# Kernel optimization log

Measured on AMD Instinct MI355X. Metric: run time of the kernel, lower is better.

The kernel has to match this reference:

```python
import jax, jax.numpy as jnp
import numpy as np

B, S, HID = 4, 2048, 2048
H, KV, D = 16, 4, 128
G = H // KV  # kv groups
EPS = 1e-6
SCALE = D ** -0.5


def setup_inputs() -> dict:
    key = jax.random.key(0)
    ks = jax.random.split(key, 8)
    hidden_states = jax.random.normal(ks[0], (B, S, HID), jnp.float32)
    # real RoPE tables (rotate-half convention: freqs duplicated across halves)
    inv_freq = 1.0 / (10000.0 ** (np.arange(0, D, 2, dtype=np.float32) / D))
    t = np.arange(S, dtype=np.float32)
    freqs = np.outer(t, inv_freq)                      # [S, D/2]
    emb = np.concatenate([freqs, freqs], axis=-1)      # [S, D]
    cos = jnp.asarray(np.cos(emb), jnp.float32)
    sin = jnp.asarray(np.sin(emb), jnp.float32)
    std = HID ** -0.5
    Wq = jax.random.normal(ks[1], (HID, H * D), jnp.float32) * std
    Wk = jax.random.normal(ks[2], (HID, KV * D), jnp.float32) * std
    Wv = jax.random.normal(ks[3], (HID, KV * D), jnp.float32) * std
    Wo = jax.random.normal(ks[4], (H * D, HID), jnp.float32) * std
    q_norm_w = jnp.ones((D,), jnp.float32)
    k_norm_w = jnp.ones((D,), jnp.float32)
    return {"hidden_states": hidden_states, "cos": cos, "sin": sin,
            "Wq": Wq, "Wk": Wk, "Wv": Wv, "Wo": Wo,
            "q_norm_w": q_norm_w, "k_norm_w": k_norm_w}


def _rms_norm(x, w):
    xf = x.astype(jnp.float32)
    var = jnp.mean(xf * xf, axis=-1, keepdims=True)
    return w * (xf * jax.lax.rsqrt(var + EPS)).astype(x.dtype)


def _rotate_half(x):
    x1, x2 = x[..., : D // 2], x[..., D // 2:]
    return jnp.concatenate([-x2, x1], axis=-1)


def reference(hidden_states, cos, sin, Wq, Wk, Wv, Wo, q_norm_w, k_norm_w):
    x = hidden_states  # [B, S, HID]
    # projections + per-head RMSNorm
    q = _rms_norm((x @ Wq).reshape(B, S, H, D), q_norm_w).transpose(0, 2, 1, 3)   # [B,H,S,D]
    k = _rms_norm((x @ Wk).reshape(B, S, KV, D), k_norm_w).transpose(0, 2, 1, 3)  # [B,KV,S,D]
    v = (x @ Wv).reshape(B, S, KV, D).transpose(0, 2, 1, 3)                        # [B,KV,S,D]
    # RoPE (cos/sin broadcast [S,D] -> [B,heads,S,D])
    q = q * cos + _rotate_half(q) * sin
    k = k * cos + _rotate_half(k) * sin
    # GQA attention without materializing expanded K/V: group q heads per kv head
    qg = q.reshape(B, KV, G, S, D)
    scores = jnp.einsum('bkgsd,bktd->bkgst', qg, k) * SCALE       # [B,KV,G,S,S]
    probs = jax.nn.softmax(scores, axis=-1)
    out = jnp.einsum('bkgst,bktd->bkgsd', probs, v)               # [B,KV,G,S,D]
    out = out.reshape(B, H, S, D).transpose(0, 2, 1, 3).reshape(B, S, H * D)
    return out @ Wo
```

## Files before the change

### kernel.cpp

```cpp
#include <hip/hip_runtime.h>

#define DEVI __device__ __forceinline__

#define B_    4
#define S_    2048
#define HID_  2048
#define H_    16
#define KV_   4
#define D_    128
#define NQKV_ 3072
#define SCALE_ 0.08838834764831845f
#define L2E_   1.44269504088896340736f

typedef __bf16 bf16x8 __attribute__((ext_vector_type(8)));
typedef float  f32x4  __attribute__((ext_vector_type(4)));
typedef unsigned short ushort_t;

DEVI unsigned short f2bu(float f) {
  unsigned u = __float_as_uint(f);
  u += 0x7fffu + ((u >> 16) & 1u);
  return (unsigned short)(u >> 16);
}
DEVI float bu2f(unsigned short s) { return __uint_as_float(((unsigned)s) << 16); }

DEVI void storev(ushort_t* p, float v) { *p = f2bu(v); }
DEVI void storev(float* p, float v)    { *p = v; }

DEVI void gl_lds16(const void* gptr, void* ldsptr) {
  __builtin_amdgcn_global_load_lds(
      (const __attribute__((address_space(1))) void*)gptr,
      (__attribute__((address_space(3))) void*)ldsptr, 16, 0, 0);
}

__global__ void k_cvt(const float* __restrict__ in, ushort_t* __restrict__ out, int n8) {
  int i = blockIdx.x * blockDim.x + threadIdx.x;
  if (i >= n8) return;
  const float4* p = (const float4*)in + (size_t)i * 2;
  float4 a = p[0], b = p[1];
  uint4 o;
  o.x = (unsigned)f2bu(a.x) | ((unsigned)f2bu(a.y) << 16);
  o.y = (unsigned)f2bu(a.z) | ((unsigned)f2bu(a.w) << 16);
  o.z = (unsigned)f2bu(b.x) | ((unsigned)f2bu(b.y) << 16);
  o.w = (unsigned)f2bu(b.z) | ((unsigned)f2bu(b.w) << 16);
  ((uint4*)out)[i] = o;
}

__global__ void k_transw(const float* __restrict__ in, ushort_t* __restrict__ out,
                         int K, int N) {
  __shared__ float tile[64][65];
  int k0 = blockIdx.x * 64, n0 = blockIdx.y * 64;
  int c = threadIdx.x & 63, r0 = threadIdx.x >> 6;
  #pragma unroll
  for (int i = 0; i < 16; ++i) {
    int r = r0 * 16 + i;
    tile[r][c] = in[(size_t)(k0 + r) * N + n0 + c];
  }
  __syncthreads();
  #pragma unroll
  for (int i = 0; i < 16; ++i) {
    int r = r0 * 16 + i;
    out[(size_t)(n0 + r) * K + k0 + c] = f2bu(tile[c][r]);
  }
}

template <typename OutT>
__global__ __launch_bounds__(256)
void k_gemm(const ushort_t* __restrict__ A, const ushort_t* __restrict__ Bt,
            OutT* __restrict__ C, int M, int N, int K) {
  __shared__ __align__(16) ushort_t As[128 * 64];
  __shared__ __align__(16) ushort_t Bs[128 * 64];
  const int tid = threadIdx.x;
  const int wave = tid >> 6, lane = tid & 63;
  const int wr = wave >> 1, wc = wave & 1;
  const int h4 = lane >> 4, c16 = lane & 15;
  const int m0 = blockIdx.x * 128, n0 = blockIdx.y * 128;

  const int srow  = wave * 8 + (lane >> 3);
  const int scolb = (lane & 7) * 16;

  const ushort_t* Ap = A  + (size_t)m0 * K;
  const ushort_t* Bp = Bt + (size_t)n0 * K;

  f32x4 acc[4][4] = {};

  for (int kt = 0; kt < K; kt += 64) {
    __syncthreads();
    #pragma unroll
    for (int p = 0; p < 4; ++p) {
      int row = p * 32 + srow;
      gl_lds16((const char*)(Ap + (size_t)row * K + kt) + scolb,
               (char*)As + p * 4096 + wave * 1024);
      gl_lds16((const char*)(Bp + (size_t)row * K + kt) + scolb,
               (char*)Bs + p * 4096 + wave * 1024);
    }
    __syncthreads();
    #pragma unroll
    for (int kc = 0; kc < 2; ++kc) {
      bf16x8 af[4], bfr[4];
      #pragma unroll
      for (int m = 0; m < 4; ++m)
        af[m] = *(const bf16x8*)((const char*)As + (wr * 64 + m * 16 + c16) * 128 + kc * 64 + h4 * 16);
      #pragma unroll
      for (int n = 0; n < 4; ++n)
        bfr[n] = *(const bf16x8*)((const char*)Bs + (wc * 64 + n * 16 + c16) * 128 + kc * 64 + h4 * 16);
      #pragma unroll
      for (int m = 0; m < 4; ++m)
        #pragma unroll
        for (int n = 0; n < 4; ++n)
          acc[m][n] = __builtin_amdgcn_mfma_f32_16x16x32_bf16(af[m], bfr[n], acc[m][n], 0, 0, 0);
    }
  }
  #pragma unroll
  for (int m = 0; m < 4; ++m)
    #pragma unroll
    for (int n = 0; n < 4; ++n)
      #pragma unroll
      for (int r = 0; r < 4; ++r) {
        int grow = m0 + wr * 64 + m * 16 + h4 * 4 + r;
        int gcol = n0 + wc * 64 + n * 16 + c16;
        storev(&C[(size_t)grow * N + gcol], acc[m][n][r]);
      }
}

__global__ void k_normrope(const ushort_t* __restrict__ qkv,
                           const float* __restrict__ cosT, const float* __restrict__ sinT,
                           const float* __restrict__ qw, const float* __restrict__ kw,
                           ushort_t* __restrict__ Qr,
                           ushort_t* __restrict__ Kr,
                           ushort_t* __restrict__ Vt) {
  int wid = blockIdx.x * 4 + (threadIdx.x >> 6);
  int lane = threadIdx.x & 63;
  int sub = wid % 24;
  int bs = wid / 24;
  int b = bs >> 11, s = bs & 2047;
  if (sub < 20) {
    bool isQ = sub < 16;
    int head = isQ ? sub : sub - 16;
    const ushort_t* rp = qkv + (size_t)bs * NQKV_ + (isQ ? head * 128 : 2048 + head * 128);
    float e0 = bu2f(rp[lane]);
    float e1 = bu2f(rp[lane + 64]);
    float ss2 = e0 * e0 + e1 * e1;
    #pragma unroll
    for (int off = 32; off; off >>= 1) ss2 += __shfl_xor(ss2, off);
    float rinv = rsqrtf(ss2 * (1.0f / 128.0f) + 1e-6f);
    const float* w = isQ ? qw : kw;
    float y0 = e0 * rinv * w[lane];
    float y1 = e1 * rinv * w[lane + 64];
    float c0 = cosT[s * 128 + lane],      sn0 = sinT[s * 128 + lane];
    float c1 = cosT[s * 128 + lane + 64], sn1 = sinT[s * 128 + lane + 64];
    float o0 = y0 * c0 - y1 * sn0;
    float o1 = y1 * c1 + y0 * sn1;
    if (isQ) { o0 *= SCALE_; o1 *= SCALE_; }
    ushort_t* op = isQ ? (Qr + ((size_t)(b * H_ + head) * S_ + s) * D_)
                       : (Kr + ((size_t)(b * KV_ + head) * S_ + s) * D_);
    op[lane]      = f2bu(o0);
    op[lane + 64] = f2bu(o1);
  } else {
    int vh = sub - 20;
    const ushort_t* rp = qkv + (size_t)bs * NQKV_ + 2560 + vh * 128;
    ushort_t* op = Vt + ((size_t)(b * KV_ + vh) * D_) * S_ + s;
    op[(size_t)lane * S_]        = rp[lane];
    op[(size_t)(lane + 64) * S_] = rp[lane + 64];
  }
}

__global__ __launch_bounds__(256)
void k_attn(const ushort_t* __restrict__ Qr, const ushort_t* __restrict__ Kr,
            const ushort_t* __restrict__ Vt, ushort_t* __restrict__ AO) {
  __shared__ __align__(16) ushort_t Ks[64 * 128];
  __shared__ __align__(16) ushort_t Vs[128 * 64];
  __shared__ __align__(16) ushort_t Ps[4][16 * 64];
  const int bh = blockIdx.y;
  const int b = bh >> 4, h = bh & 15, kvh = h >> 2;
  const int q0 = blockIdx.x * 64;
  const int tid = threadIdx.x;
  const int wave = tid >> 6, lane = tid & 63;
  const int h4 = lane >> 4, c16 = lane & 15;

  const ushort_t* qp = Qr + ((size_t)(b * H_ + h) * S_ + q0 + wave * 16 + c16) * D_;
  bf16x8 qf[4];
  #pragma unroll
  for (int kc = 0; kc < 4; ++kc)
    qf[kc] = *(const bf16x8*)(qp + kc * 32 + h4 * 8);

  const ushort_t* Kg = Kr + (size_t)(b * KV_ + kvh) * S_ * D_;
  const ushort_t* Vg = Vt + (size_t)(b * KV_ + kvh) * D_ * S_;

  float mrow = -1e30f, lsum = 0.0f;
  f32x4 Of[8] = {};
  ushort_t* pw = &Ps[wave][0];
  const int xq = (c16 & 7) << 4;

  for (int nt = 0; nt < S_ / 64; ++nt) {
    const int s0 = nt * 64;
    __syncthreads();
    #pragma unroll
    for (int p = 0; p < 4; ++p) {
      int off = p * 4096 + wave * 1024 + lane * 16;
      {
        int row = off >> 8, colb = off & 255;
        int sc = colb ^ ((row & 7) << 4);
        gl_lds16((const char*)(Kg + (size_t)(s0 + row) * D_) + sc,
                 (char*)Ks + p * 4096 + wave * 1024);
      }
      {
        int row = off >> 7, colb = off & 127;
        int sc = colb ^ ((row & 7) << 4);
        gl_lds16((const char*)(Vg + (size_t)row * S_ + s0) + sc,
                 (char*)Vs + p * 4096 + wave * 1024);
      }
    }
    __syncthreads();

    f32x4 st[4] = {};
    #pragma unroll
    for (int kvt = 0; kvt < 4; ++kvt) {
      const int krow = kvt * 16 + c16;
      const int xr = (krow & 7) << 4;
      #pragma unroll
      for (int kc = 0; kc < 4; ++kc) {
        bf16x8 kf = *(const bf16x8*)((const char*)Ks + krow * 256 + ((kc * 64 + h4 * 16) ^ xr));
        st[kvt] = __builtin_amdgcn_mfma_f32_16x16x32_bf16(kf, qf[kc], st[kvt], 0, 0, 0);
      }
    }

    float tmax = -1e30f;
    #pragma unroll
    for (int kvt = 0; kvt < 4; ++kvt)
      #pragma unroll
      for (int r = 0; r < 4; ++r) tmax = fmaxf(tmax, st[kvt][r]);
    tmax = fmaxf(tmax, __shfl_xor(tmax, 16));
    tmax = fmaxf(tmax, __shfl_xor(tmax, 32));
    const float mnew = fmaxf(mrow, tmax);
    const float corr = exp2f((mrow - mnew) * L2E_);
    mrow = mnew;

    float psum = 0.0f;
    #pragma unroll
    for (int kvt = 0; kvt < 4; ++kvt)
      #pragma unroll
      for (int r = 0; r < 4; ++r) {
        float pv = exp2f((st[kvt][r] - mnew) * L2E_);
        psum += pv;
        int kvi = kvt * 16 + h4 * 4 + r;
        *(ushort_t*)((char*)pw + c16 * 128 + ((kvi * 2) ^ xq)) = f2bu(pv);
      }
    lsum = lsum * corr + psum;

    float cr[4];
    #pragma unroll
    for (int r = 0; r < 4; ++r) cr[r] = __shfl(corr, (lane & 48) + h4 * 4 + r);
    #pragma unroll
    for (int dt = 0; dt < 8; ++dt)
      #pragma unroll
      for (int r = 0; r < 4; ++r) Of[dt][r] *= cr[r];

    #pragma unroll
    for (int kvc = 0; kvc < 2; ++kvc) {
      bf16x8 pa = *(const bf16x8*)((const char*)pw + c16 * 128 + ((kvc * 64 + h4 * 16) ^ xq));
      #pragma unroll
      for (int dt = 0; dt < 8; ++dt) {
        const int vrow = dt * 16 + c16;
        bf16x8 vb = *(const bf16x8*)((const char*)Vs + vrow * 128 +
                                     ((kvc * 64 + h4 * 16) ^ ((vrow & 7) << 4)));
        Of[dt] = __builtin_amdgcn_mfma_f32_16x16x32_bf16(pa, vb, Of[dt], 0, 0, 0);
      }
    }
  }

  lsum += __shfl_xor(lsum, 16);
  lsum += __shfl_xor(lsum, 32);
  const float inv = 1.0f / lsum;
  float invr[4];
  #pragma unroll
  for (int r = 0; r < 4; ++r) invr[r] = __shfl(inv, (lane & 48) + h4 * 4 + r);

  #pragma unroll
  for (int dt = 0; dt < 8; ++dt)
    #pragma unroll
    for (int r = 0; r < 4; ++r) {
      const int s = q0 + wave * 16 + h4 * 4 + r;
      AO[((size_t)(b * S_ + s) * H_ + h) * D_ + dt * 16 + c16] = f2bu(Of[dt][r] * invr[r]);
    }
}

extern "C" void kernel_launch(void* const* d_in, const int* in_sizes, int n_in,
                              void* d_out, int out_size, void* d_ws, size_t ws_size,
                              hipStream_t stream) {
  const float* x    = (const float*)d_in[0];
  const float* cosT = (const float*)d_in[1];
  const float* sinT = (const float*)d_in[2];
  const float* Wq   = (const float*)d_in[3];
  const float* Wk   = (const float*)d_in[4];
  const float* Wv   = (const float*)d_in[5];
  const float* Wo   = (const float*)d_in[6];
  const float* qw   = (const float*)d_in[7];
  const float* kw   = (const float*)d_in[8];
  float* out = (float*)d_out;

  char* ws = (char*)d_ws;
  ushort_t* Xb    = (ushort_t*)(ws + 0);
  ushort_t* QKVt  = (ushort_t*)(ws + 33554432);
  ushort_t* Wtqkv = (ushort_t*)(ws + 83886080);
  ushort_t* Wto   = (ushort_t*)(ws + 96468992);
  ushort_t* Kr    = (ushort_t*)(ws + 104857600);
  ushort_t* Vt    = (ushort_t*)(ws + 113246208);
  ushort_t* Qr = Xb;
  ushort_t* AO = QKVt;

  k_cvt<<<8192, 256, 0, stream>>>(x, Xb, 2097152);
  k_transw<<<dim3(32, 32), 256, 0, stream>>>(Wq, Wtqkv, 2048, 2048);
  k_transw<<<dim3(32, 8),  256, 0, stream>>>(Wk, Wtqkv + (size_t)2048 * 2048, 2048, 512);
  k_transw<<<dim3(32, 8),  256, 0, stream>>>(Wv, Wtqkv + (size_t)2560 * 2048, 2048, 512);
  k_transw<<<dim3(32, 32), 256, 0, stream>>>(Wo, Wto, 2048, 2048);
  k_gemm<ushort_t><<<dim3(64, 24), 256, 0, stream>>>(Xb, Wtqkv, QKVt, 8192, 3072, 2048);
  k_normrope<<<49152, 256, 0, stream>>>(QKVt, cosT, sinT, qw, kw, Qr, Kr, Vt);
  k_attn<<<dim3(32, 64), 256, 0, stream>>>(Qr, Kr, Vt, AO);
  k_gemm<float><<<dim3(64, 16), 256, 0, stream>>>(AO, Wto, out, 8192, 2048, 2048);
}
```

Measured before the change: 755.9 us.

## Double-buffer attention K/V tiles, keep P in registers, tile V transpose

The attention kernel now double-buffers K and V tiles in LDS, prefetching the next tile while computing on the current one, with one barrier per iteration instead of two. P probabilities are packed into bf16 pairs and redistributed across lanes with shuffles instead of a round trip through LDS. The MFMA operand order is swapped so that per-row correction and normalisation need no shuffles, which also gives packed output stores. The strided scalar V transpose in normrope moves to a separate LDS-tiled transpose kernel. This adds LDS usage and extra shuffle instructions in exchange for less global-memory latency exposure and fewer scattered writes.

```diff
diff --git a/kernel.cpp b/kernel.cpp
--- a/kernel.cpp
+++ b/kernel.cpp
@@ -22,6 +22,9 @@
   return (unsigned short)(u >> 16);
 }
 DEVI float bu2f(unsigned short s) { return __uint_as_float(((unsigned)s) << 16); }
+DEVI unsigned pk2(float a, float b) {
+  return (unsigned)f2bu(a) | ((unsigned)f2bu(b) << 16);
+}
 
 DEVI void storev(ushort_t* p, float v) { *p = f2bu(v); }
 DEVI void storev(float* p, float v)    { *p = v; }
@@ -38,10 +41,10 @@
   const float4* p = (const float4*)in + (size_t)i * 2;
   float4 a = p[0], b = p[1];
   uint4 o;
-  o.x = (unsigned)f2bu(a.x) | ((unsigned)f2bu(a.y) << 16);
-  o.y = (unsigned)f2bu(a.z) | ((unsigned)f2bu(a.w) << 16);
-  o.z = (unsigned)f2bu(b.x) | ((unsigned)f2bu(b.y) << 16);
-  o.w = (unsigned)f2bu(b.z) | ((unsigned)f2bu(b.w) << 16);
+  o.x = pk2(a.x, a.y);
+  o.y = pk2(a.z, a.w);
+  o.z = pk2(b.x, b.y);
+  o.w = pk2(b.z, b.w);
   ((uint4*)out)[i] = o;
 }
 
@@ -60,6 +63,26 @@
   for (int i = 0; i < 16; ++i) {
     int r = r0 * 16 + i;
     out[(size_t)(n0 + r) * K + k0 + c] = f2bu(tile[c][r]);
+  }
+}
+
+__global__ void k_vtrans(const ushort_t* __restrict__ qkv, ushort_t* __restrict__ Vt) {
+  __shared__ ushort_t tile[64][65];
+  int s0 = blockIdx.x * 64, d0 = blockIdx.y * 64;
+  int bkv = blockIdx.z, b = bkv >> 2, vh = bkv & 3;
+  int c = threadIdx.x & 63, r0 = (threadIdx.x >> 6) * 16;
+  const ushort_t* src = qkv + (size_t)(b * S_ + s0) * NQKV_ + 2560 + vh * 128 + d0;
+  #pragma unroll
+  for (int i = 0; i < 16; ++i) {
+    int r = r0 + i;
+    tile[r][c] = src[(size_t)r * NQKV_ + c];
+  }
+  __syncthreads();
+  ushort_t* dst = Vt + ((size_t)(b * KV_ + vh) * D_ + d0) * S_ + s0;
+  #pragma unroll
+  for (int i = 0; i < 16; ++i) {
+    int r = r0 + i;
+    dst[(size_t)r * S_ + c] = tile[c][r];
   }
 }
 
@@ -126,50 +149,40 @@
                            const float* __restrict__ cosT, const float* __restrict__ sinT,
                            const float* __restrict__ qw, const float* __restrict__ kw,
                            ushort_t* __restrict__ Qr,
-                           ushort_t* __restrict__ Kr,
-                           ushort_t* __restrict__ Vt) {
+                           ushort_t* __restrict__ Kr) {
   int wid = blockIdx.x * 4 + (threadIdx.x >> 6);
   int lane = threadIdx.x & 63;
-  int sub = wid % 24;
-  int bs = wid / 24;
+  int sub = wid % 20;
+  int bs = wid / 20;
   int b = bs >> 11, s = bs & 2047;
-  if (sub < 20) {
-    bool isQ = sub < 16;
-    int head = isQ ? sub : sub - 16;
-    const ushort_t* rp = qkv + (size_t)bs * NQKV_ + (isQ ? head * 128 : 2048 + head * 128);
-    float e0 = bu2f(rp[lane]);
-    float e1 = bu2f(rp[lane + 64]);
-    float ss2 = e0 * e0 + e1 * e1;
-    #pragma unroll
-    for (int off = 32; off; off >>= 1) ss2 += __shfl_xor(ss2, off);
-    float rinv = rsqrtf(ss2 * (1.0f / 128.0f) + 1e-6f);
-    const float* w = isQ ? qw : kw;
-    float y0 = e0 * rinv * w[lane];
-    float y1 = e1 * rinv * w[lane + 64];
-    float c0 = cosT[s * 128 + lane],      sn0 = sinT[s * 128 + lane];
-    float c1 = cosT[s * 128 + lane + 64], sn1 = sinT[s * 128 + lane + 64];
-    float o0 = y0 * c0 - y1 * sn0;
-    float o1 = y1 * c1 + y0 * sn1;
-    if (isQ) { o0 *= SCALE_; o1 *= SCALE_; }
-    ushort_t* op = isQ ? (Qr + ((size_t)(b * H_ + head) * S_ + s) * D_)
-                       : (Kr + ((size_t)(b * KV_ + head) * S_ + s) * D_);
-    op[lane]      = f2bu(o0);
-    op[lane + 64] = f2bu(o1);
-  } else {
-    int vh = sub - 20;
-    const ushort_t* rp = qkv + (size_t)bs * NQKV_ + 2560 + vh * 128;
-    ushort_t* op = Vt + ((size_t)(b * KV_ + vh) * D_) * S_ + s;
-    op[(size_t)lane * S_]        = rp[lane];
-    op[(size_t)(lane + 64) * S_] = rp[lane + 64];
-  }
+  bool isQ = sub < 16;
+  int head = isQ ? sub : sub - 16;
+  const ushort_t* rp = qkv + (size_t)bs * NQKV_ + (isQ ? head * 128 : 2048 + head * 128);
+  float e0 = bu2f(rp[lane]);
+  float e1 = bu2f(rp[lane + 64]);
+  float ss2 = e0 * e0 + e1 * e1;
+  #pragma unroll
+  for (int off = 32; off; off >>= 1) ss2 += __shfl_xor(ss2, off);
+  float rinv = rsqrtf(ss2 * (1.0f / 128.0f) + 1e-6f);
+  const float* w = isQ ? qw : kw;
+  float y0 = e0 * rinv * w[lane];
+  float y1 = e1 * rinv * w[lane + 64];
+  float c0 = cosT[s * 128 + lane],      sn0 = sinT[s * 128 + lane];
+  float c1 = cosT[s * 128 + lane + 64], sn1 = sinT[s * 128 + lane + 64];
+  float o0 = y0 * c0 - y1 * sn0;
+  float o1 = y1 * c1 + y0 * sn1;
+  if (isQ) { o0 *= SCALE_; o1 *= SCALE_; }
+  ushort_t* op = isQ ? (Qr + ((size_t)(b * H_ + head) * S_ + s) * D_)
+                     : (Kr + ((size_t)(b * KV_ + head) * S_ + s) * D_);
+  op[lane]      = f2bu(o0);
+  op[lane + 64] = f2bu(o1);
 }
 
 __global__ __launch_bounds__(256)
 void k_attn(const ushort_t* __restrict__ Qr, const ushort_t* __restrict__ Kr,
             const ushort_t* __restrict__ Vt, ushort_t* __restrict__ AO) {
-  __shared__ __align__(16) ushort_t Ks[64 * 128];
-  __shared__ __align__(16) ushort_t Vs[128 * 64];
-  __shared__ __align__(16) ushort_t Ps[4][16 * 64];
+  __shared__ __align__(16) ushort_t Ks[2][64 * 128];
+  __shared__ __align__(16) ushort_t Vs[2][64 * 128];
   const int bh = blockIdx.y;
   const int b = bh >> 4, h = bh & 15, kvh = h >> 2;
   const int q0 = blockIdx.x * 64;
@@ -186,31 +199,38 @@
   const ushort_t* Kg = Kr + (size_t)(b * KV_ + kvh) * S_ * D_;
   const ushort_t* Vg = Vt + (size_t)(b * KV_ + kvh) * D_ * S_;
 
+  const int soff = wave * 1024 + lane * 16;
+
   float mrow = -1e30f, lsum = 0.0f;
   f32x4 Of[8] = {};
-  ushort_t* pw = &Ps[wave][0];
-  const int xq = (c16 & 7) << 4;
+
+#define STAGE(bufi, s0)                                                        \
+  {                                                                            \
+    _Pragma("unroll")                                                          \
+    for (int p = 0; p < 4; ++p) {                                              \
+      int off = p * 4096 + soff;                                               \
+      int krow = off >> 8, kcolb = off & 255;                                  \
+      int ksc = kcolb ^ ((krow & 7) << 4);                                     \
+      gl_lds16((const char*)(Kg + (size_t)((s0) + krow) * D_) + ksc,           \
+               (char*)Ks[bufi] + p * 4096 + wave * 1024);                      \
+      int vrow = off >> 7, vcolb = off & 127;                                  \
+      int vsc = vcolb ^ ((vrow & 7) << 4);                                     \
+      gl_lds16((const char*)(Vg + (size_t)vrow * S_ + (s0)) + vsc,             \
+               (char*)Vs[bufi] + p * 4096 + wave * 1024);                      \
+    }                                                                          \
+  }
+
+  STAGE(0, 0);
+  asm volatile("s_waitcnt vmcnt(0)" ::: "memory");
+  __builtin_amdgcn_s_barrier();
+
+  const int srcA = (2 * (h4 & 1)) * 16 + c16;
+  const int srcB = srcA + 16;
+  const bool hiKvt = (h4 >> 1) != 0;
 
   for (int nt = 0; nt < S_ / 64; ++nt) {
-    const int s0 = nt * 64;
-    __syncthreads();
-    #pragma unroll
-    for (int p = 0; p < 4; ++p) {
-      int off = p * 4096 + wave * 1024 + lane * 16;
-      {
-        int row = off >> 8, colb = off & 255;
-        int sc = colb ^ ((row & 7) << 4);
-        gl_lds16((const char*)(Kg + (size_t)(s0 + row) * D_) + sc,
-                 (char*)Ks + p * 4096 + wave * 1024);
-      }
-      {
-        int row = off >> 7, colb = off & 127;
-        int sc = colb ^ ((row & 7) << 4);
-        gl_lds16((const char*)(Vg + (size_t)row * S_ + s0) + sc,
-                 (char*)Vs + p * 4096 + wave * 1024);
-      }
-    }
-    __syncthreads();
+    const int cur = nt & 1;
+    if (nt + 1 < S_ / 64) STAGE(cur ^ 1, (nt + 1) * 64);
 
     f32x4 st[4] = {};
     #pragma unroll
@@ -219,7 +239,8 @@
       const int xr = (krow & 7) << 4;
       #pragma unroll
       for (int kc = 0; kc < 4; ++kc) {
-        bf16x8 kf = *(const bf16x8*)((const char*)Ks + krow * 256 + ((kc * 64 + h4 * 16) ^ xr));
+        bf16x8 kf = *(const bf16x8*)((const char*)Ks[cur] + krow * 256 +
+                                     ((kc * 64 + h4 * 16) ^ xr));
         st[kvt] = __builtin_amdgcn_mfma_f32_16x16x32_bf16(kf, qf[kc], st[kvt], 0, 0, 0);
       }
     }
@@ -236,52 +257,62 @@
     mrow = mnew;
 
     float psum = 0.0f;
-    #pragma unroll
-    for (int kvt = 0; kvt < 4; ++kvt)
-      #pragma unroll
-      for (int r = 0; r < 4; ++r) {
-        float pv = exp2f((st[kvt][r] - mnew) * L2E_);
-        psum += pv;
-        int kvi = kvt * 16 + h4 * 4 + r;
-        *(ushort_t*)((char*)pw + c16 * 128 + ((kvi * 2) ^ xq)) = f2bu(pv);
-      }
+    unsigned pu[4][2];
+    #pragma unroll
+    for (int kvt = 0; kvt < 4; ++kvt) {
+      float p0 = exp2f((st[kvt][0] - mnew) * L2E_);
+      float p1 = exp2f((st[kvt][1] - mnew) * L2E_);
+      float p2 = exp2f((st[kvt][2] - mnew) * L2E_);
+      float p3 = exp2f((st[kvt][3] - mnew) * L2E_);
+      psum += (p0 + p1) + (p2 + p3);
+      pu[kvt][0] = pk2(p0, p1);
+      pu[kvt][1] = pk2(p2, p3);
+    }
     lsum = lsum * corr + psum;
 
-    float cr[4];
-    #pragma unroll
-    for (int r = 0; r < 4; ++r) cr[r] = __shfl(corr, (lane & 48) + h4 * 4 + r);
     #pragma unroll
     for (int dt = 0; dt < 8; ++dt)
       #pragma unroll
-      for (int r = 0; r < 4; ++r) Of[dt][r] *= cr[r];
+      for (int r = 0; r < 4; ++r) Of[dt][r] *= corr;
 
     #pragma unroll
     for (int kvc = 0; kvc < 2; ++kvc) {
-      bf16x8 pa = *(const bf16x8*)((const char*)pw + c16 * 128 + ((kvc * 64 + h4 * 16) ^ xq));
+      unsigned w0a = __shfl(pu[kvc * 2][0], srcA), w0b = __shfl(pu[kvc * 2 + 1][0], srcA);
+      unsigned w1a = __shfl(pu[kvc * 2][1], srcA), w1b = __shfl(pu[kvc * 2 + 1][1], srcA);
+      unsigned w2a = __shfl(pu[kvc * 2][0], srcB), w2b = __shfl(pu[kvc * 2 + 1][0], srcB);
+      unsigned w3a = __shfl(pu[kvc * 2][1], srcB), w3b = __shfl(pu[kvc * 2 + 1][1], srcB);
+      uint4 pw;
+      pw.x = hiKvt ? w0b : w0a;
+      pw.y = hiKvt ? w1b : w1a;
+      pw.z = hiKvt ? w2b : w2a;
+      pw.w = hiKvt ? w3b : w3a;
+      bf16x8 pb = __builtin_bit_cast(bf16x8, pw);
       #pragma unroll
       for (int dt = 0; dt < 8; ++dt) {
         const int vrow = dt * 16 + c16;
-        bf16x8 vb = *(const bf16x8*)((const char*)Vs + vrow * 128 +
+        bf16x8 vb = *(const bf16x8*)((const char*)Vs[cur] + vrow * 128 +
                                      ((kvc * 64 + h4 * 16) ^ ((vrow & 7) << 4)));
-        Of[dt] = __builtin_amdgcn_mfma_f32_16x16x32_bf16(pa, vb, Of[dt], 0, 0, 0);
+        Of[dt] = __builtin_amdgcn_mfma_f32_16x16x32_bf16(vb, pb, Of[dt], 0, 0, 0);
       }
     }
-  }
+
+    asm volatile("s_waitcnt vmcnt(0)" ::: "memory");
+    __builtin_amdgcn_s_barrier();
+  }
+#undef STAGE
 
   lsum += __shfl_xor(lsum, 16);
   lsum += __shfl_xor(lsum, 32);
   const float inv = 1.0f / lsum;
-  float invr[4];
-  #pragma unroll
-  for (int r = 0; r < 4; ++r) invr[r] = __shfl(inv, (lane & 48) + h4 * 4 + r);
-
-  #pragma unroll
-  for (int dt = 0; dt < 8; ++dt)
-    #pragma unroll
-    for (int r = 0; r < 4; ++r) {
-      const int s = q0 + wave * 16 + h4 * 4 + r;
-      AO[((size_t)(b * S_ + s) * H_ + h) * D_ + dt * 16 + c16] = f2bu(Of[dt][r] * invr[r]);
-    }
+
+  const int s = q0 + wave * 16 + c16;
+  ushort_t* aop = AO + ((size_t)(b * S_ + s) * H_ + h) * D_;
+  #pragma unroll
+  for (int dt = 0; dt < 8; ++dt) {
+    const int d0 = dt * 16 + h4 * 4;
+    *(unsigned*)(aop + d0)     = pk2(Of[dt][0] * inv, Of[dt][1] * inv);
+    *(unsigned*)(aop + d0 + 2) = pk2(Of[dt][2] * inv, Of[dt][3] * inv);
+  }
 }
 
 extern "C" void kernel_launch(void* const* d_in, const int* in_sizes, int n_in,
@@ -314,7 +345,8 @@
   k_transw<<<dim3(32, 8),  256, 0, stream>>>(Wv, Wtqkv + (size_t)2560 * 2048, 2048, 512);
   k_transw<<<dim3(32, 32), 256, 0, stream>>>(Wo, Wto, 2048, 2048);
   k_gemm<ushort_t><<<dim3(64, 24), 256, 0, stream>>>(Xb, Wtqkv, QKVt, 8192, 3072, 2048);
-  k_normrope<<<49152, 256, 0, stream>>>(QKVt, cosT, sinT, qw, kw, Qr, Kr, Vt);
+  k_normrope<<<40960, 256, 0, stream>>>(QKVt, cosT, sinT, qw, kw, Qr, Kr);
+  k_vtrans<<<dim3(32, 2, 16), 256, 0, stream>>>(QKVt, Vt);
   k_attn<<<dim3(32, 64), 256, 0, stream>>>(Qr, Kr, Vt, AO);
   k_gemm<float><<<dim3(64, 16), 256, 0, stream>>>(AO, Wto, out, 8192, 2048, 2048);
 }
```

Measured after the change: 741.5 us. About the same (-1.9%).
